# Optimization experiments

Measured on AMD Instinct MI355X. Metric: run time of the kernel, lower is better.

Reference implementation:

```python
import jax, jax.numpy as jnp
import numpy as np

BATCH, SEQ = 4, 2048
D_MODEL, INNER, STATE, K, FFN = 384, 768, 16, 4, 1024


def setup_inputs() -> dict:
    key = jax.random.key(0)
    ks = jax.random.split(key, 12)
    def g(k, shape, scale=0.02):
        return jax.random.normal(k, shape, jnp.float32) * scale
    return {
        "x": jax.random.normal(ks[0], (BATCH, SEQ, D_MODEL), jnp.float32),
        "rms1_w": jnp.ones((D_MODEL,), jnp.float32),
        "rms2_w": jnp.ones((D_MODEL,), jnp.float32),
        "in_proj_w": g(ks[1], (D_MODEL, 2 * INNER)),
        "conv_w": g(ks[2], (K, INNER, INNER)),
        "conv_b": jnp.zeros((INNER,), jnp.float32),
        "x_proj_w": g(ks[3], (INNER, 2 * STATE)),
        "dt_proj_w": g(ks[4], (INNER, INNER)),
        "dt_proj_b": jnp.zeros((INNER,), jnp.float32),
        "A_log": jnp.log(jax.random.uniform(ks[5], (INNER, STATE), jnp.float32, 1.0, 16.0)),
        "D_param": jnp.ones((INNER,), jnp.float32),
        "out_proj_w": g(ks[6], (INNER, D_MODEL)),
        "ln_gamma": jnp.ones((D_MODEL,), jnp.float32),
        "ln_beta": jnp.zeros((D_MODEL,), jnp.float32),
        "gate_w": g(ks[7], (D_MODEL, FFN)),
        "up_w": g(ks[8], (D_MODEL, FFN)),
        "down_w": g(ks[9], (FFN, D_MODEL)),
    }


def rms_norm(x, w, eps=1e-6):
    norm = jnp.sqrt(jnp.mean(jnp.square(x), axis=-1, keepdims=True) + eps)
    return x / norm * w


def layer_norm(x, gamma, beta, eps=1e-5):
    mu = jnp.mean(x, axis=-1, keepdims=True)
    var = jnp.mean(jnp.square(x - mu), axis=-1, keepdims=True)
    return (x - mu) / jnp.sqrt(var + eps) * gamma + beta


def selective_scan(x, delta, A_log, Bm, Cm, Dp):
    # x, delta: [B,L,Di]; Bm, Cm: [B,L,N]; A_log: [Di,N]; Dp: [Di]
    delta = jax.nn.softplus(delta)
    A = -jnp.exp(A_log)                          # [Di,N]
    A_disc = jnp.exp(delta[..., None] * A)       # [B,L,Di,N]
    B_disc = delta[..., None] * Bm[:, :, None, :]  # [B,L,Di,N]
    xs = jnp.moveaxis(x, 1, 0)       # [L,B,Di]
    As = jnp.moveaxis(A_disc, 1, 0)  # [L,B,Di,N]
    Bs = jnp.moveaxis(B_disc, 1, 0)  # [L,B,Di,N]
    Cs = jnp.moveaxis(Cm, 1, 0)      # [L,B,N]
    h0 = jnp.zeros((x.shape[0], A_log.shape[0], A_log.shape[1]), x.dtype)
    def step(h, inp):
        x_t, A_t, B_t, C_t = inp
        h = A_t * h + B_t * x_t[..., None]          # [B,Di,N]
        y_t = jnp.einsum('bdn,bn->bd', h, C_t)      # [B,Di]
        return h, y_t
    _, ys = jax.lax.scan(step, h0, (xs, As, Bs, Cs))
    y = jnp.moveaxis(ys, 0, 1)       # [B,L,Di]
    return y + Dp * x


def mamba_core(h, in_proj_w, conv_w, conv_b, x_proj_w, dt_proj_w, dt_proj_b,
               A_log, D_param, out_proj_w, ln_gamma, ln_beta):
    xz = h @ in_proj_w                             # [B,L,2*Di]
    x_inner, z = jnp.split(xz, 2, axis=-1)
    # Conv1D SAME padding (k=4 -> pad (1,2)), channels-last, kernel [W,I,O]
    x_conv = jax.lax.conv_general_dilated(
        x_inner, conv_w, window_strides=(1,), padding='SAME',
        dimension_numbers=('NWC', 'WIO', 'NWC')) + conv_b
    x_conv = jax.nn.silu(x_conv)
    Bm, Cm = jnp.split(x_conv @ x_proj_w, 2, axis=-1)  # each [B,L,N]
    delta = x_conv @ dt_proj_w + dt_proj_b            # [B,L,Di]
    y = selective_scan(x_conv, delta, A_log, Bm, Cm, D_param)
    y = y * jax.nn.silu(z)
    out = y @ out_proj_w
    return layer_norm(out, ln_gamma, ln_beta)


def reference(x, rms1_w, rms2_w, in_proj_w, conv_w, conv_b, x_proj_w,
              dt_proj_w, dt_proj_b, A_log, D_param, out_proj_w, ln_gamma,
              ln_beta, gate_w, up_w, down_w):
    residual = x
    h = rms_norm(x, rms1_w)
    h = mamba_core(h, in_proj_w, conv_w, conv_b, x_proj_w, dt_proj_w,
                   dt_proj_b, A_log, D_param, out_proj_w, ln_gamma, ln_beta)
    x = residual + h  # dropout inactive (training=False)
    residual = x
    h = rms_norm(x, rms2_w)
    hidden = jax.nn.silu(h @ gate_w) * (h @ up_w)
    x = residual + hidden @ down_w
    return x
```

## Files before the change

### kernel.cpp

```cpp
#include <hip/hip_runtime.h>
#include <hip/hip_bf16.h>


using u16 = unsigned short;
using u32 = unsigned int;
using short8 = __attribute__((ext_vector_type(8))) short;
using f32x4  = __attribute__((ext_vector_type(4))) float;

#define TTOK 8192
#define DM 384
#define DI 768
#define NST 16
#define LSEQ 2048
#define NCH 64
#define LCH 32

#define SWZ_R(row, quad) \
  ((row) * 32 + ((((quad) ^ (row) ^ ((row) >> 2)) & 3) * 8))
#define SWZ_W(tid) SWZ_R((tid) >> 2, (tid) & 3)

__device__ __forceinline__ float bf2f(u16 a) {
  u32 u = ((u32)a) << 16;
  float f; __builtin_memcpy(&f, &u, 4); return f;
}
__device__ __forceinline__ u16 f2bf(float f) {
  u32 u; __builtin_memcpy(&u, &f, 4);
  u32 r = (u + 0x7fffu + ((u >> 16) & 1u)) >> 16;
  return (u16)r;
}
__device__ __forceinline__ int probe_bf(const void* rw) {
  return (((const u32*)rw)[0] == 0x3F803F80u) ? 1 : 0;
}
__device__ __forceinline__ float ld_in(const void* p, int i, int isbf) {
  return isbf ? bf2f(((const u16*)p)[i]) : ((const float*)p)[i];
}
__device__ __forceinline__ float fexp2(float x) {
#if __has_builtin(__builtin_amdgcn_exp2f)
  return __builtin_amdgcn_exp2f(x);
#else
  return exp2f(x);
#endif
}
__device__ __forceinline__ float wave_sum(float v) {
#pragma unroll
  for (int off = 32; off > 0; off >>= 1) v += __shfl_xor(v, off, 64);
  return v;
}

#define V_CB 0
#define V_DB 768
#define V_DP 1536
#define V_R1 2304
#define V_R2 2688
#define V_GA 3072
#define V_BE 3456

__global__ __launch_bounds__(256) void k_prep(
    const void* __restrict__ x, const void* __restrict__ in_proj,
    const void* __restrict__ conv_w, const void* __restrict__ dt_w,
    const void* __restrict__ x_proj, const void* __restrict__ out_proj,
    const void* __restrict__ gate_w, const void* __restrict__ up_w,
    const void* __restrict__ down_w, const void* __restrict__ A_log,
    const void* __restrict__ conv_b, const void* __restrict__ dt_b,
    const void* __restrict__ Dp, const void* __restrict__ rms1_w,
    const void* __restrict__ rms2_w, const void* __restrict__ gamma,
    const void* __restrict__ beta,
    u16* __restrict__ W1T, u16* __restrict__ WCT, u16* __restrict__ W45T,
    u16* __restrict__ W5T, u16* __restrict__ W6T, u16* __restrict__ W7T,
    float* __restrict__ An2T, u16* __restrict__ vecs,
    u16* __restrict__ WinX, u16* __restrict__ h1pad) {
  const int isbf = probe_bf(rms1_w);
  const int bx = blockIdx.x;
  const int tid = threadIdx.x;
  __shared__ u16 lt[64 * 66];

  if (bx < 1236) {
    const void* src; size_t soff = 0; u16* dst; int R, C, tpr, lo;
    if (bx < 144)       { src = in_proj;  dst = W1T;  R = 384;  C = 1536; tpr = 24; lo = bx; }
    else if (bx < 720)  { int tp = (bx - 144) / 144; lo = (bx - 144) % 144;
                          src = conv_w; soff = (size_t)tp * 589824;
                          dst = WCT + (size_t)tp * 589824; R = 768; C = 768; tpr = 12; }
    else if (bx < 864)  { src = dt_w;     dst = W45T; R = 768;  C = 768;  tpr = 12; lo = bx - 720; }
    else if (bx < 876)  { src = x_proj;   dst = W45T + (size_t)768 * 768;
                          R = 768; C = 32; tpr = 1; lo = bx - 864; }
    else if (bx < 948)  { src = out_proj; dst = W5T;  R = 768;  C = 384;  tpr = 6;  lo = bx - 876; }
    else if (bx < 1044) { src = gate_w;   dst = W6T;  R = 384;  C = 1024; tpr = 16; lo = bx - 948; }
    else if (bx < 1140) { src = up_w;     dst = W6T + (size_t)1024 * 384;
                          R = 384; C = 1024; tpr = 16; lo = bx - 1044; }
    else                { src = down_w;   dst = W7T;  R = 1024; C = 384;  tpr = 6;  lo = bx - 1140; }
    int tr = lo / tpr, tc = lo % tpr;
    int r0 = tr * 64, c0 = tc * 64;
#pragma unroll
    for (int i = 0; i < 16; ++i) {
      int el = i * 256 + tid, lr = el >> 6, lc = el & 63;
      if (c0 + lc < C)
        lt[lr * 66 + lc] =
            f2bf(ld_in(src, (int)(soff + (size_t)(r0 + lr) * C + c0 + lc), isbf));
    }
    __syncthreads();
#pragma unroll
    for (int i = 0; i < 16; ++i) {
      int el = i * 256 + tid, orow = el >> 6, oc = el & 63;
      if (c0 + orow < C)
        dst[(size_t)(c0 + orow) * R + r0 + oc] = lt[oc * 66 + orow];
    }
    return;
  }
  if (bx < 5332) {
    int half = tid >> 7;
    int t = (bx - 1236) * 2 + half;
    int tid2 = tid & 127;
    int lane = tid & 63, wv = tid >> 6;
    float v[3]; float q = 0.f;
#pragma unroll
    for (int j = 0; j < 3; ++j) {
      v[j] = ld_in(x, t * DM + tid2 + j * 128, isbf);
      q += v[j] * v[j];
    }
    q = wave_sum(q);
    float* rq = (float*)lt;
    if (lane == 0) rq[wv] = q;
    __syncthreads();
    float rr = rsqrtf((rq[half * 2] + rq[half * 2 + 1]) * (1.f / DM) + 1e-6f);
    int b = t >> 11, l = t & 2047;
    size_t orow = ((size_t)(b * 2051 + l + 1)) * DM;
#pragma unroll
    for (int j = 0; j < 3; ++j) {
      int i = tid2 + j * 128;
      h1pad[orow + i] = f2bf(v[j] * rr * ld_in(rms1_w, i, isbf));
    }
    return;
  }
  if (bx < 6484) {
    int lo = (bx - 5332) * 256 + tid;
    int i = lo / 768, j = lo % 768;
    WinX[lo] = f2bf(ld_in(in_proj, i * 1536 + j, isbf));
    return;
  }
  if (bx < 6532) {
    int lo = (bx - 6484) * 256 + tid;
    if (lo < 12288) {
      int d = lo >> 4, n = lo & 15;
      An2T[n * DI + d] = -__expf(ld_in(A_log, lo, isbf)) * 1.44269504f;
    }
    return;
  }
  if (bx < 6547) {
    int lo = (bx - 6532) * 256 + tid;
    if (lo < 3840) {
      const void* s; int o;
      if      (lo < 768)  { s = conv_b; o = lo; }
      else if (lo < 1536) { s = dt_b;   o = lo - 768; }
      else if (lo < 2304) { s = Dp;     o = lo - 1536; }
      else if (lo < 2688) { s = rms1_w; o = lo - 2304; }
      else if (lo < 3072) { s = rms2_w; o = lo - 2688; }
      else if (lo < 3456) { s = gamma;  o = lo - 3072; }
      else                { s = beta;   o = lo - 3456; }
      vecs[lo] = f2bf(ld_in(s, o, isbf));
    }
    return;
  }
  {
    int lo = (bx - 6547) * 256 + tid;
    if (lo < 4608) {
      int b = lo / (3 * DM), rem = lo % (3 * DM);
      int which = rem / DM, i = rem % DM;
      int row = b * 2051 + (which == 0 ? 0 : (2048 + which));
      h1pad[(size_t)row * DM + i] = 0;
    }
  }
}

__global__ __launch_bounds__(128) void k_lnrms(const float* __restrict__ outm,
                                               const void* __restrict__ xin,
                                               const void* __restrict__ rw,
                                               const u16* __restrict__ vecs,
                                               float* __restrict__ x2f,
                                               u16* __restrict__ h2) {
  const int isbf = probe_bf(rw);
  int t = blockIdx.x, tid = threadIdx.x;
  int lane = tid & 63, wid = tid >> 6;
  float v[3]; float s = 0.f, q = 0.f;
#pragma unroll
  for (int j = 0; j < 3; ++j) {
    v[j] = outm[(size_t)t * DM + tid + j * 128];
    s += v[j]; q += v[j] * v[j];
  }
  s = wave_sum(s); q = wave_sum(q);
  __shared__ float rs[2], rq[2], r2[2];
  if (lane == 0) { rs[wid] = s; rq[wid] = q; }
  __syncthreads();
  float mu = (rs[0] + rs[1]) * (1.f / DM);
  float var = (rq[0] + rq[1]) * (1.f / DM) - mu * mu;
  float rstd = rsqrtf(var + 1e-5f);
  float x2v[3]; float q2 = 0.f;
#pragma unroll
  for (int j = 0; j < 3; ++j) {
    int i = tid + j * 128;
    float ln = (v[j] - mu) * rstd * bf2f(vecs[V_GA + i]) + bf2f(vecs[V_BE + i]);
    x2v[j] = ld_in(xin, t * DM + i, isbf) + ln;
    x2f[(size_t)t * DM + i] = x2v[j];
    q2 += x2v[j] * x2v[j];
  }
  q2 = wave_sum(q2);
  if (lane == 0) r2[wid] = q2;
  __syncthreads();
  float rr = rsqrtf((r2[0] + r2[1]) * (1.f / DM) + 1e-6f);
#pragma unroll
  for (int j = 0; j < 3; ++j) {
    int i = tid + j * 128;
    h2[(size_t)t * DM + i] = f2bf(x2v[j] * rr * bf2f(vecs[V_R2 + i]));
  }
}

template <int EPI, int MT, int NT, int KDIM>
__global__ __launch_bounds__(256) void gemm_bt(
    const u16* __restrict__ A, const u16* __restrict__ BT,
    float* __restrict__ o1, float* __restrict__ o2,
    u16* __restrict__ ob1, u16* __restrict__ ob2,
    const u16* __restrict__ bias, const float* __restrict__ res,
    const void* __restrict__ fl) {
  constexpr int AFR = MT / 32, BFR = NT / 32;
  __shared__ u16 smem[MT * 64 + NT * 64];
  const int tid = threadIdx.x;
  const int lane = tid & 63, wid = tid >> 6;
  const int wm = (wid >> 1) * (MT / 2), wn = (wid & 1) * (NT / 2);
  const int fr = lane & 15, quad = lane >> 4;
  const int r0 = tid >> 2, c8 = (tid & 3) << 3;
  const int m0 = blockIdx.x * MT, n0 = blockIdx.y * NT;

  f32x4 acc[AFR][BFR] = {};

  const u16* BTe = (EPI == 6) ? BT + (size_t)blockIdx.z * 589824 : BT;
  const u16* gB0 = BTe + (size_t)(n0 + r0) * KDIM + c8;
  const u16* gA0 = A + (size_t)(m0 + r0) * KDIM + c8;

  short8 a00, a01, a10, a11, b00, b01, b10, b11;
  auto stage_load = [&](int kt) {
    a00 = *(const short8*)(gA0 + kt);
    a10 = *(const short8*)(gA0 + kt + 32);
    if (MT == 128) {
      a01 = *(const short8*)(gA0 + kt + (size_t)64 * KDIM);
      a11 = *(const short8*)(gA0 + kt + 32 + (size_t)64 * KDIM);
    }
    b00 = *(const short8*)(gB0 + kt);
    b10 = *(const short8*)(gB0 + kt + 32);
    if (NT == 128) {
      b01 = *(const short8*)(gB0 + kt + (size_t)64 * KDIM);
      b11 = *(const short8*)(gB0 + kt + 32 + (size_t)64 * KDIM);
    }
  };

  stage_load(0);

#pragma unroll 1
  for (int kt = 0; kt < KDIM; kt += 64) {
    __syncthreads();
    *(short8*)&smem[SWZ_W(tid)] = a00;
    if (MT == 128) *(short8*)&smem[2048 + SWZ_W(tid)] = a01;
    *(short8*)&smem[MT * 32 + SWZ_W(tid)] = a10;
    if (MT == 128) *(short8*)&smem[MT * 32 + 2048 + SWZ_W(tid)] = a11;
    *(short8*)&smem[MT * 64 + SWZ_W(tid)] = b00;
    if (NT == 128) *(short8*)&smem[MT * 64 + 2048 + SWZ_W(tid)] = b01;
    *(short8*)&smem[MT * 64 + NT * 32 + SWZ_W(tid)] = b10;
    if (NT == 128) *(short8*)&smem[MT * 64 + NT * 32 + 2048 + SWZ_W(tid)] = b11;
    __syncthreads();
    if (kt + 64 < KDIM) stage_load(kt + 64);
#pragma unroll
    for (int kh = 0; kh < 2; ++kh) {
      const int ao = kh * MT * 32, bo = MT * 64 + kh * NT * 32;
      short8 af[AFR], bfg[BFR];
#pragma unroll
      for (int i = 0; i < AFR; ++i)
        af[i] = *(const short8*)&smem[ao + SWZ_R(wm + i * 16 + fr, quad)];
#pragma unroll
      for (int i = 0; i < BFR; ++i)
        bfg[i] = *(const short8*)&smem[bo + SWZ_R(wn + i * 16 + fr, quad)];
#pragma unroll
      for (int mt = 0; mt < AFR; ++mt)
#pragma unroll
        for (int nt = 0; nt < BFR; ++nt)
          acc[mt][nt] = __builtin_amdgcn_mfma_f32_16x16x32_bf16(
              af[mt], bfg[nt], acc[mt][nt], 0, 0, 0);
    }
  }

  int isbf = 0;
  if (EPI == 5) isbf = probe_bf(fl);

#pragma unroll
  for (int mt = 0; mt < AFR; ++mt) {
#pragma unroll
    for (int nt = 0; nt < BFR; ++nt) {
#pragma unroll
      for (int r = 0; r < 4; ++r) {
        int t = m0 + wm + mt * 16 + quad * 4 + r;
        int n = n0 + wn + nt * 16 + fr;
        float v = acc[mt][nt][r];
        if (EPI == 2) {
          if (n < DI) {
            float xx = v + bf2f(bias[n]);
            float sp = (xx > 20.f) ? xx : log1pf(__expf(xx));
            ob1[(size_t)t * DI + n] = f2bf(sp);
          } else if (n < DI + 32) {
            o2[(size_t)t * 32 + (n - DI)] = v;
          }
        } else if (EPI == 3) {
          o1[(size_t)t * DM + n] = v;
        } else if (EPI == 5) {
          float val = v + res[(size_t)t * DM + n];
          if (isbf) ob1[(size_t)t * DM + n] = f2bf(val);
          else      o1[(size_t)t * DM + n] = val;
        } else if (EPI == 6) {
          ob1[(size_t)n * 1536 + blockIdx.z * 384 + t] = f2bf(v);
        }
      }
    }
  }
}

__global__ __launch_bounds__(256) void gemm_xz(
    const u16* __restrict__ A, const u16* __restrict__ WC,
    const u16* __restrict__ WZ, u16* __restrict__ xconv,
    u16* __restrict__ zbuf, const u16* __restrict__ bias) {
  __shared__ u16 smem[8192];
  const int tid = threadIdx.x;
  const int lane = tid & 63, wid = tid >> 6;
  const int wm = (wid >> 1) << 5, wn = (wid & 1) << 5;
  const int fr = lane & 15, quad = lane >> 4;
  const int r0 = tid >> 2, c8 = (tid & 3) << 3;
  const int yb = blockIdx.y;
  const bool isz = yb >= 12;
  const int kd = isz ? 384 : 1536;
  const u16* BT = isz ? WZ : WC;
  const int kldb = isz ? 384 : 1536;
  const int n0 = (isz ? yb - 12 : yb) * 64;
  const int m0 = blockIdx.x * 64;

  f32x4 acc[2][2] = {};

  const u16* gB0 = BT + (size_t)(n0 + r0) * kldb + c8;
  const int b = m0 >> 11, l0 = m0 & 2047;
  const u16* gA0 = A + (size_t)(b * 2051 + l0 + r0 + (isz ? 1 : 0)) * DM + c8;

  short8 a0, a1, b0, b1;
  int wconv = 0, i0 = 0;
  auto calcA = [&]() -> const u16* {
    const u16* p = gA0 + (size_t)wconv * DM + i0;
    i0 += 32;
    if (i0 == DM) { i0 = 0; ++wconv; }
    return p;
  };
  auto stage_load = [&](int kt) {
    a0 = *(const short8*)calcA();
    a1 = *(const short8*)calcA();
    b0 = *(const short8*)(gB0 + kt);
    b1 = *(const short8*)(gB0 + kt + 32);
  };

  stage_load(0);

#pragma unroll 1
  for (int kt = 0; kt < kd; kt += 64) {
    __syncthreads();
    *(short8*)&smem[SWZ_W(tid)]        = a0;
    *(short8*)&smem[2048 + SWZ_W(tid)] = a1;
    *(short8*)&smem[4096 + SWZ_W(tid)] = b0;
    *(short8*)&smem[6144 + SWZ_W(tid)] = b1;
    __syncthreads();
    if (kt + 64 < kd) stage_load(kt + 64);
#pragma unroll
    for (int kh = 0; kh < 2; ++kh) {
      const int ao = kh * 2048, bo = 4096 + kh * 2048;
      short8 af[2], bfg[2];
#pragma unroll
      for (int i = 0; i < 2; ++i)
        af[i] = *(const short8*)&smem[ao + SWZ_R(wm + i * 16 + fr, quad)];
#pragma unroll
      for (int i = 0; i < 2; ++i)
        bfg[i] = *(const short8*)&smem[bo + SWZ_R(wn + i * 16 + fr, quad)];
#pragma unroll
      for (int mt = 0; mt < 2; ++mt)
#pragma unroll
        for (int nt = 0; nt < 2; ++nt)
          acc[mt][nt] = __builtin_amdgcn_mfma_f32_16x16x32_bf16(
              af[mt], bfg[nt], acc[mt][nt], 0, 0, 0);
    }
  }

#pragma unroll
  for (int mt = 0; mt < 2; ++mt) {
#pragma unroll
    for (int nt = 0; nt < 2; ++nt) {
#pragma unroll
      for (int r = 0; r < 4; ++r) {
        int t = m0 + wm + mt * 16 + quad * 4 + r;
        int n = n0 + wn + nt * 16 + fr;
        float v = acc[mt][nt][r];
        if (isz) {
          zbuf[(size_t)t * DI + n] = f2bf(v);
        } else {
          float xx = v + bf2f(bias[n]);
          float sg = 1.f / (1.f + __expf(-xx));
          xconv[(size_t)t * DI + n] = f2bf(xx * sg);
        }
      }
    }
  }
}

__global__ __launch_bounds__(256) void gemm_gu(
    const u16* __restrict__ A, const u16* __restrict__ W6T,
    u16* __restrict__ hid) {
  __shared__ u16 smem[12288];
  const int tid = threadIdx.x;
  const int lane = tid & 63, wid = tid >> 6;
  const int wm = (wid >> 1) << 5, wn = (wid & 1) << 5;
  const int fr = lane & 15, quad = lane >> 4;
  const int r0 = tid >> 2, c8 = (tid & 3) << 3;
  const int m0 = blockIdx.x * 64, n0 = blockIdx.y * 64;

  f32x4 accg[2][2] = {}, accu[2][2] = {};

  const u16* gA0 = A + (size_t)(m0 + r0) * DM + c8;
  const u16* gG0 = W6T + (size_t)(n0 + r0) * DM + c8;
  const u16* gU0 = W6T + (size_t)(1024 + n0 + r0) * DM + c8;

  short8 a0, a1, g00, g10, u00, u10;
  auto stage_load = [&](int kt) {
    a0  = *(const short8*)(gA0 + kt);
    a1  = *(const short8*)(gA0 + kt + 32);
    g00 = *(const short8*)(gG0 + kt);
    g10 = *(const short8*)(gG0 + kt + 32);
    u00 = *(const short8*)(gU0 + kt);
    u10 = *(const short8*)(gU0 + kt + 32);
  };

  stage_load(0);

#pragma unroll 1
  for (int kt = 0; kt < DM; kt += 64) {
    __syncthreads();
    *(short8*)&smem[SWZ_W(tid)]          = a0;
    *(short8*)&smem[2048 + SWZ_W(tid)]   = a1;
    *(short8*)&smem[4096 + SWZ_W(tid)]   = g00;
    *(short8*)&smem[6144 + SWZ_W(tid)]   = g10;
    *(short8*)&smem[8192 + SWZ_W(tid)]   = u00;
    *(short8*)&smem[10240 + SWZ_W(tid)]  = u10;
    __syncthreads();
    if (kt + 64 < DM) stage_load(kt + 64);
#pragma unroll
    for (int kh = 0; kh < 2; ++kh) {
      const int ao = kh * 2048, go = 4096 + kh * 2048, uo = 8192 + kh * 2048;
      short8 af[2], bg[2], bu[2];
#pragma unroll
      for (int i = 0; i < 2; ++i)
        af[i] = *(const short8*)&smem[ao + SWZ_R(wm + i * 16 + fr, quad)];
#pragma unroll
      for (int i = 0; i < 2; ++i) {
        bg[i] = *(const short8*)&smem[go + SWZ_R(wn + i * 16 + fr, quad)];
        bu[i] = *(const short8*)&smem[uo + SWZ_R(wn + i * 16 + fr, quad)];
      }
#pragma unroll
      for (int mt = 0; mt < 2; ++mt)
#pragma unroll
        for (int nt = 0; nt < 2; ++nt) {
          accg[mt][nt] = __builtin_amdgcn_mfma_f32_16x16x32_bf16(
              af[mt], bg[nt], accg[mt][nt], 0, 0, 0);
          accu[mt][nt] = __builtin_amdgcn_mfma_f32_16x16x32_bf16(
              af[mt], bu[nt], accu[mt][nt], 0, 0, 0);
        }
    }
  }

#pragma unroll
  for (int mt = 0; mt < 2; ++mt) {
#pragma unroll
    for (int nt = 0; nt < 2; ++nt) {
#pragma unroll
      for (int r = 0; r < 4; ++r) {
        int t = m0 + wm + mt * 16 + quad * 4 + r;
        int n = n0 + wn + nt * 16 + fr;
        float g = accg[mt][nt][r];
        float u = accu[mt][nt][r];
        float sg = 1.f / (1.f + __expf(-g));
        hid[(size_t)t * 1024 + n] = f2bf(g * sg * u);
      }
    }
  }
}

__global__ __launch_bounds__(256) void k_scan1(
    const u16* __restrict__ deltab, const u16* __restrict__ xconv,
    const float* __restrict__ BC, const float* __restrict__ An2T,
    float* __restrict__ hlb, float* __restrict__ Pb) {
  int gid = blockIdx.x * 256 + threadIdx.x;
  int d = gid % DI, bc = gid / DI, c = bc & (NCH - 1), b = bc >> 6;
  float An[NST];
#pragma unroll
  for (int n = 0; n < NST; ++n) An[n] = An2T[n * DI + d];
  float h[NST], P[NST];
#pragma unroll
  for (int n = 0; n < NST; ++n) { h[n] = 0.f; P[n] = 1.f; }
  int row0 = b * LSEQ + c * LCH;
  float dt = bf2f(deltab[(size_t)row0 * DI + d]);
  float xv = bf2f(xconv[(size_t)row0 * DI + d]);
  float4 q[4];
  {
    const float4* q4 = (const float4*)(BC + (size_t)row0 * 32);
#pragma unroll
    for (int i = 0; i < 4; ++i) q[i] = q4[i];
  }
  for (int s = 0; s < LCH; ++s) {
    float dtc = dt, xvc = xv;
    float Bm[NST];
#pragma unroll
    for (int i = 0; i < 4; ++i) {
      Bm[4*i] = q[i].x; Bm[4*i+1] = q[i].y;
      Bm[4*i+2] = q[i].z; Bm[4*i+3] = q[i].w;
    }
    if (s + 1 < LCH) {
      int r2 = row0 + s + 1;
      dt = bf2f(deltab[(size_t)r2 * DI + d]);
      xv = bf2f(xconv[(size_t)r2 * DI + d]);
      const float4* q4 = (const float4*)(BC + (size_t)r2 * 32);
#pragma unroll
      for (int i = 0; i < 4; ++i) q[i] = q4[i];
    }
    float dxv = dtc * xvc;
#pragma unroll
    for (int n = 0; n < NST; ++n) {
      float a = fexp2(dtc * An[n]);
      h[n] = fmaf(a, h[n], dxv * Bm[n]);
      P[n] *= a;
    }
  }
  float4* ph = (float4*)(hlb + (size_t)gid * NST);
  float4* pp = (float4*)(Pb + (size_t)gid * NST);
#pragma unroll
  for (int i = 0; i < 4; ++i) {
    ph[i] = make_float4(h[4*i], h[4*i+1], h[4*i+2], h[4*i+3]);
    pp[i] = make_float4(P[4*i], P[4*i+1], P[4*i+2], P[4*i+3]);
  }
}

__global__ __launch_bounds__(256) void k_scan2(const float* __restrict__ hlb,
                                               const float* __restrict__ Pb,
                                               float* __restrict__ hin) {
  int gid = blockIdx.x * 256 + threadIdx.x;
  int n = gid & 15, bd = gid >> 4;
  int d = bd % DI, b = bd / DI;
  float H = 0.f;
  for (int c = 0; c < NCH; ++c) {
    size_t idx = ((size_t)((b * NCH + c) * DI + d)) * NST + n;
    hin[idx] = H;
    H = hlb[idx] + Pb[idx] * H;
  }
}

__global__ __launch_bounds__(256) void k_scan3(
    const u16* __restrict__ deltab, const u16* __restrict__ xconv,
    const float* __restrict__ BC, const float* __restrict__ An2T,
    const float* __restrict__ hinb, const u16* __restrict__ zb,
    const u16* __restrict__ vecs, u16* __restrict__ ys) {
  int gid = blockIdx.x * 256 + threadIdx.x;
  int d = gid % DI, bc = gid / DI, c = bc & (NCH - 1), b = bc >> 6;
  float An[NST];
#pragma unroll
  for (int n = 0; n < NST; ++n) An[n] = An2T[n * DI + d];
  float h[NST];
  {
    const float4* hp = (const float4*)(hinb + (size_t)gid * NST);
#pragma unroll
    for (int i = 0; i < 4; ++i) {
      float4 t = hp[i];
      h[4*i] = t.x; h[4*i+1] = t.y; h[4*i+2] = t.z; h[4*i+3] = t.w;
    }
  }
  float Dd = bf2f(vecs[V_DP + d]);
  int row0 = b * LSEQ + c * LCH;
  float dt = bf2f(deltab[(size_t)row0 * DI + d]);
  float xv = bf2f(xconv[(size_t)row0 * DI + d]);
  float zv = bf2f(zb[(size_t)row0 * DI + d]);
  float4 q[8];
  {
    const float4* q4 = (const float4*)(BC + (size_t)row0 * 32);
#pragma unroll
    for (int i = 0; i < 8; ++i) q[i] = q4[i];
  }
  for (int s = 0; s < LCH; ++s) {
    int row = row0 + s;
    float dtc = dt, xvc = xv, zvc = zv;
    float Bm[NST], Cm[NST];
#pragma unroll
    for (int i = 0; i < 4; ++i) {
      Bm[4*i] = q[i].x;   Bm[4*i+1] = q[i].y;
      Bm[4*i+2] = q[i].z; Bm[4*i+3] = q[i].w;
      Cm[4*i] = q[4+i].x;   Cm[4*i+1] = q[4+i].y;
      Cm[4*i+2] = q[4+i].z; Cm[4*i+3] = q[4+i].w;
    }
    if (s + 1 < LCH) {
      int r2 = row + 1;
      dt = bf2f(deltab[(size_t)r2 * DI + d]);
      xv = bf2f(xconv[(size_t)r2 * DI + d]);
      zv = bf2f(zb[(size_t)r2 * DI + d]);
      const float4* q4 = (const float4*)(BC + (size_t)r2 * 32);
#pragma unroll
      for (int i = 0; i < 8; ++i) q[i] = q4[i];
    }
    float dxv = dtc * xvc;
    float yp[4] = {0.f, 0.f, 0.f, 0.f};
#pragma unroll
    for (int n = 0; n < NST; ++n) {
      float a = fexp2(dtc * An[n]);
      h[n] = fmaf(a, h[n], dxv * Bm[n]);
      yp[n & 3] = fmaf(h[n], Cm[n], yp[n & 3]);
    }
    float y = (yp[0] + yp[1]) + (yp[2] + yp[3]);
    float sz = zvc / (1.f + __expf(-zvc));
    ys[(size_t)row * DI + d] = f2bf((y + Dd * xvc) * sz);
  }
}

extern "C" void kernel_launch(void* const* d_in, const int* in_sizes, int n_in,
                              void* d_out, int out_size, void* d_ws,
                              size_t ws_size, hipStream_t stream) {
  (void)in_sizes; (void)n_in; (void)out_size;
  const void* x        = d_in[0];
  const void* rms1_w   = d_in[1];
  const void* rms2_w   = d_in[2];
  const void* in_proj  = d_in[3];
  const void* conv_w   = d_in[4];
  const void* conv_b   = d_in[5];
  const void* x_proj   = d_in[6];
  const void* dt_w     = d_in[7];
  const void* dt_b     = d_in[8];
  const void* A_log    = d_in[9];
  const void* Dp       = d_in[10];
  const void* out_proj = d_in[11];
  const void* gamma    = d_in[12];
  const void* beta     = d_in[13];
  const void* gate_w   = d_in[14];
  const void* up_w     = d_in[15];
  const void* down_w   = d_in[16];

  char* ws = (char*)d_ws;
  size_t off = 0;
  auto alloc = [&](size_t bytes) -> void* {
    void* p = ws + off;
    off = (off + bytes + 255) & ~(size_t)255;
    return p;
  };
  u16*   W1T   = (u16*)alloc((size_t)1536 * 384 * 2);
  u16*   WCT   = (u16*)alloc((size_t)4 * 768 * 768 * 2);
  u16*   W45T  = (u16*)alloc((size_t)896 * 768 * 2);
  u16*   W5T   = (u16*)alloc((size_t)384 * 768 * 2);
  u16*   W6T   = (u16*)alloc((size_t)2048 * 384 * 2);
  u16*   W7T   = (u16*)alloc((size_t)384 * 1024 * 2);
  float* An2T  = (float*)alloc((size_t)16 * 768 * 4);
  u16*   vecs  = (u16*)alloc(3840 * 2);
  u16*   WinX  = (u16*)alloc((size_t)384 * 768 * 2);
  u16*   WcombT= (u16*)alloc((size_t)768 * 1536 * 2);
  u16*   h1pad = (u16*)alloc((size_t)4 * 2051 * 384 * 2);
  u16*   zbuf  = (u16*)alloc((size_t)8192 * 768 * 2);
  u16*   xconv = (u16*)alloc((size_t)8192 * 768 * 2);
  u16*   deltab= (u16*)alloc((size_t)8192 * 768 * 2);
  float* BCb   = (float*)alloc((size_t)8192 * 32 * 4);
  float* hl    = (float*)alloc((size_t)196608 * 16 * 4);
  float* Pb    = (float*)alloc((size_t)196608 * 16 * 4);
  float* hin   = (float*)alloc((size_t)196608 * 16 * 4);
  u16*   ys   = (u16*)hl;
  float* outm = Pb;
  float* x2f  = hin;
  u16*   h2   = h1pad;
  u16*   hid  = (u16*)hl;

  if (off > ws_size) return;

  k_prep<<<6565, 256, 0, stream>>>(
      x, in_proj, conv_w, dt_w, x_proj, out_proj, gate_w, up_w, down_w,
      A_log, conv_b, dt_b, Dp, rms1_w, rms2_w, gamma, beta,
      W1T, WCT, W45T, W5T, W6T, W7T, An2T, vecs, WinX, h1pad);

  gemm_bt<6, 64, 64, 768><<<dim3(6, 12, 4), 256, 0, stream>>>(
      WinX, WCT, nullptr, nullptr, WcombT, nullptr, nullptr, nullptr, nullptr);

  gemm_xz<<<dim3(128, 24), 256, 0, stream>>>(
      h1pad, WcombT, W1T + (size_t)768 * 384, xconv, zbuf, vecs + V_CB);

  gemm_bt<2, 64, 64, 768><<<dim3(128, 13), 256, 0, stream>>>(
      xconv, W45T, nullptr, BCb, deltab, nullptr, vecs + V_DB, nullptr,
      nullptr);

  k_scan1<<<768, 256, 0, stream>>>(deltab, xconv, BCb, An2T, hl, Pb);
  k_scan2<<<192, 256, 0, stream>>>(hl, Pb, hin);
  k_scan3<<<768, 256, 0, stream>>>(deltab, xconv, BCb, An2T, hin, zbuf, vecs,
                                   ys);

  gemm_bt<3, 64, 64, 768><<<dim3(128, 6), 256, 0, stream>>>(
      ys, W5T, outm, nullptr, nullptr, nullptr, nullptr, nullptr, nullptr);
  k_lnrms<<<8192, 128, 0, stream>>>(outm, x, rms1_w, vecs, x2f, h2);

  gemm_gu<<<dim3(128, 16), 256, 0, stream>>>(h2, W6T, hid);
  gemm_bt<5, 64, 64, 1024><<<dim3(128, 6), 256, 0, stream>>>(
      hid, W7T, (float*)d_out, nullptr, (u16*)d_out, nullptr, nullptr, x2f,
      rms1_w);
}
```

Measured before the change: 323.8 us.

## Use direct global-to-LDS loads with double-buffered shared memory in GEMMs

Replaces the register-staged global loads in gemm_bt and gemm_xz with global_load_lds DMA-style copies straight into LDS, and double-buffers shared memory so the next tile loads while the current one is consumed. This drops one __syncthreads per k-step and the VGPR round-trip for staging data. It doubles LDS use per block and relies on the swizzle computed on the source side plus implicit wait semantics; there is no explicit vmcnt wait before the barrier, which could be a correctness risk depending on compiler handling.

```diff
diff --git a/kernel.cpp b/kernel.cpp
--- a/kernel.cpp
+++ b/kernel.cpp
@@ -45,6 +45,12 @@
 #pragma unroll
   for (int off = 32; off > 0; off >>= 1) v += __shfl_xor(v, off, 64);
   return v;
+}
+
+__device__ __forceinline__ void gl_lds16(const u16* g, u16* l) {
+  __builtin_amdgcn_global_load_lds(
+      (const __attribute__((address_space(1))) u32*)g,
+      (__attribute__((address_space(3))) u32*)l, 16, 0, 0);
 }
 
 #define V_CB 0
@@ -213,85 +219,72 @@
   }
 }
 
-template <int EPI, int MT, int NT, int KDIM>
+template <int EPI, int KDIM>
 __global__ __launch_bounds__(256) void gemm_bt(
     const u16* __restrict__ A, const u16* __restrict__ BT,
     float* __restrict__ o1, float* __restrict__ o2,
     u16* __restrict__ ob1, u16* __restrict__ ob2,
     const u16* __restrict__ bias, const float* __restrict__ res,
     const void* __restrict__ fl) {
-  constexpr int AFR = MT / 32, BFR = NT / 32;
-  __shared__ u16 smem[MT * 64 + NT * 64];
+  __shared__ u16 smem[2][8192];
   const int tid = threadIdx.x;
   const int lane = tid & 63, wid = tid >> 6;
-  const int wm = (wid >> 1) * (MT / 2), wn = (wid & 1) * (NT / 2);
+  const int wm = (wid >> 1) << 5, wn = (wid & 1) << 5;
   const int fr = lane & 15, quad = lane >> 4;
-  const int r0 = tid >> 2, c8 = (tid & 3) << 3;
-  const int m0 = blockIdx.x * MT, n0 = blockIdx.y * NT;
-
-  f32x4 acc[AFR][BFR] = {};
-
+  const int m0 = blockIdx.x * 64, n0 = blockIdx.y * 64;
+
+  f32x4 acc[2][2] = {};
+
+  const int wrow = (wid << 4) | (lane >> 2);
+  const int sq = ((lane & 3) ^ wrow ^ (wrow >> 2)) & 3;
   const u16* BTe = (EPI == 6) ? BT + (size_t)blockIdx.z * 589824 : BT;
-  const u16* gB0 = BTe + (size_t)(n0 + r0) * KDIM + c8;
-  const u16* gA0 = A + (size_t)(m0 + r0) * KDIM + c8;
-
-  short8 a00, a01, a10, a11, b00, b01, b10, b11;
-  auto stage_load = [&](int kt) {
-    a00 = *(const short8*)(gA0 + kt);
-    a10 = *(const short8*)(gA0 + kt + 32);
-    if (MT == 128) {
-      a01 = *(const short8*)(gA0 + kt + (size_t)64 * KDIM);
-      a11 = *(const short8*)(gA0 + kt + 32 + (size_t)64 * KDIM);
-    }
-    b00 = *(const short8*)(gB0 + kt);
-    b10 = *(const short8*)(gB0 + kt + 32);
-    if (NT == 128) {
-      b01 = *(const short8*)(gB0 + kt + (size_t)64 * KDIM);
-      b11 = *(const short8*)(gB0 + kt + 32 + (size_t)64 * KDIM);
-    }
+  const u16* srcA = A + (size_t)(m0 + wrow) * KDIM + sq * 8;
+  const u16* srcB = BTe + (size_t)(n0 + wrow) * KDIM + sq * 8;
+  u16* lw = &smem[0][0] + (wid << 9);
+
+  auto stage = [&](int buf, int kt) {
+    u16* lb = lw + buf * 8192;
+    gl_lds16(srcA + kt,      lb);
+    gl_lds16(srcA + kt + 32, lb + 2048);
+    gl_lds16(srcB + kt,      lb + 4096);
+    gl_lds16(srcB + kt + 32, lb + 6144);
   };
 
-  stage_load(0);
+  stage(0, 0);
+  int cur = 0;
 
 #pragma unroll 1
   for (int kt = 0; kt < KDIM; kt += 64) {
     __syncthreads();
-    *(short8*)&smem[SWZ_W(tid)] = a00;
-    if (MT == 128) *(short8*)&smem[2048 + SWZ_W(tid)] = a01;
-    *(short8*)&smem[MT * 32 + SWZ_W(tid)] = a10;
-    if (MT == 128) *(short8*)&smem[MT * 32 + 2048 + SWZ_W(tid)] = a11;
-    *(short8*)&smem[MT * 64 + SWZ_W(tid)] = b00;
-    if (NT == 128) *(short8*)&smem[MT * 64 + 2048 + SWZ_W(tid)] = b01;
-    *(short8*)&smem[MT * 64 + NT * 32 + SWZ_W(tid)] = b10;
-    if (NT == 128) *(short8*)&smem[MT * 64 + NT * 32 + 2048 + SWZ_W(tid)] = b11;
-    __syncthreads();
-    if (kt + 64 < KDIM) stage_load(kt + 64);
+    if (kt + 64 < KDIM) stage(cur ^ 1, kt + 64);
+    const u16* sm = &smem[cur][0];
 #pragma unroll
     for (int kh = 0; kh < 2; ++kh) {
-      const int ao = kh * MT * 32, bo = MT * 64 + kh * NT * 32;
-      short8 af[AFR], bfg[BFR];
-#pragma unroll
-      for (int i = 0; i < AFR; ++i)
-        af[i] = *(const short8*)&smem[ao + SWZ_R(wm + i * 16 + fr, quad)];
-#pragma unroll
-      for (int i = 0; i < BFR; ++i)
-        bfg[i] = *(const short8*)&smem[bo + SWZ_R(wn + i * 16 + fr, quad)];
-#pragma unroll
-      for (int mt = 0; mt < AFR; ++mt)
-#pragma unroll
-        for (int nt = 0; nt < BFR; ++nt)
+      const int ao = kh * 2048, bo = 4096 + kh * 2048;
+      short8 af[2], bfg[2];
+#pragma unroll
+      for (int i = 0; i < 2; ++i)
+        af[i] = *(const short8*)&sm[ao + SWZ_R(wm + i * 16 + fr, quad)];
+#pragma unroll
+      for (int i = 0; i < 2; ++i)
+        bfg[i] = *(const short8*)&sm[bo + SWZ_R(wn + i * 16 + fr, quad)];
+#pragma unroll
+      for (int mt = 0; mt < 2; ++mt)
+#pragma unroll
+        for (int nt = 0; nt < 2; ++nt)
           acc[mt][nt] = __builtin_amdgcn_mfma_f32_16x16x32_bf16(
               af[mt], bfg[nt], acc[mt][nt], 0, 0, 0);
     }
+    cur ^= 1;
   }
 
   int isbf = 0;
   if (EPI == 5) isbf = probe_bf(fl);
 
 #pragma unroll
-  for (int mt = 0; mt < AFR; ++mt) {
-#pragma unroll
-    for (int nt = 0; nt < BFR; ++nt) {
+  for (int mt = 0; mt < 2; ++mt) {
+#pragma unroll
+    for (int nt = 0; nt < 2; ++nt) {
 #pragma unroll
       for (int r = 0; r < 4; ++r) {
         int t = m0 + wm + mt * 16 + quad * 4 + r;
@@ -323,12 +316,11 @@
     const u16* __restrict__ A, const u16* __restrict__ WC,
     const u16* __restrict__ WZ, u16* __restrict__ xconv,
     u16* __restrict__ zbuf, const u16* __restrict__ bias) {
-  __shared__ u16 smem[8192];
+  __shared__ u16 smem[2][8192];
   const int tid = threadIdx.x;
   const int lane = tid & 63, wid = tid >> 6;
   const int wm = (wid >> 1) << 5, wn = (wid & 1) << 5;
   const int fr = lane & 15, quad = lane >> 4;
-  const int r0 = tid >> 2, c8 = (tid & 3) << 3;
   const int yb = blockIdx.y;
   const bool isz = yb >= 12;
   const int kd = isz ? 384 : 1536;
@@ -339,46 +331,43 @@
 
   f32x4 acc[2][2] = {};
 
-  const u16* gB0 = BT + (size_t)(n0 + r0) * kldb + c8;
+  const int wrow = (wid << 4) | (lane >> 2);
+  const int sq = ((lane & 3) ^ wrow ^ (wrow >> 2)) & 3;
+  const u16* srcB = BT + (size_t)(n0 + wrow) * kldb + sq * 8;
   const int b = m0 >> 11, l0 = m0 & 2047;
-  const u16* gA0 = A + (size_t)(b * 2051 + l0 + r0 + (isz ? 1 : 0)) * DM + c8;
-
-  short8 a0, a1, b0, b1;
-  int wconv = 0, i0 = 0;
-  auto calcA = [&]() -> const u16* {
-    const u16* p = gA0 + (size_t)wconv * DM + i0;
-    i0 += 32;
-    if (i0 == DM) { i0 = 0; ++wconv; }
-    return p;
+  const u16* srcA0 =
+      A + (size_t)(b * 2051 + l0 + wrow + (isz ? 1 : 0)) * DM + sq * 8;
+  u16* lw = &smem[0][0] + (wid << 9);
+
+  int wc = 0, ic = 0;
+  auto stage = [&](int buf, int kt) {
+    u16* lb = lw + buf * 8192;
+    const u16* sa = srcA0 + (size_t)wc * DM + ic;
+    gl_lds16(sa,           lb);
+    gl_lds16(sa + 32,      lb + 2048);
+    gl_lds16(srcB + kt,      lb + 4096);
+    gl_lds16(srcB + kt + 32, lb + 6144);
+    ic += 64; if (ic == 384) { ic = 0; ++wc; }
   };
-  auto stage_load = [&](int kt) {
-    a0 = *(const short8*)calcA();
-    a1 = *(const short8*)calcA();
-    b0 = *(const short8*)(gB0 + kt);
-    b1 = *(const short8*)(gB0 + kt + 32);
-  };
-
-  stage_load(0);
+
+  stage(0, 0);
+  int cur = 0;
 
 #pragma unroll 1
   for (int kt = 0; kt < kd; kt += 64) {
     __syncthreads();
-    *(short8*)&smem[SWZ_W(tid)]        = a0;
-    *(short8*)&smem[2048 + SWZ_W(tid)] = a1;
-    *(short8*)&smem[4096 + SWZ_W(tid)] = b0;
-    *(short8*)&smem[6144 + SWZ_W(tid)] = b1;
-    __syncthreads();
-    if (kt + 64 < kd) stage_load(kt + 64);
+    if (kt + 64 < kd) stage(cur ^ 1, kt + 64);
+    const u16* sm = &smem[cur][0];
 #pragma unroll
     for (int kh = 0; kh < 2; ++kh) {
       const int ao = kh * 2048, bo = 4096 + kh * 2048;
       short8 af[2], bfg[2];
 #pragma unroll
       for (int i = 0; i < 2; ++i)
-        af[i] = *(const short8*)&smem[ao + SWZ_R(wm + i * 16 + fr, quad)];
+        af[i] = *(const short8*)&sm[ao + SWZ_R(wm + i * 16 + fr, quad)];
 #pragma unroll
       for (int i = 0; i < 2; ++i)
-        bfg[i] = *(const short8*)&smem[bo + SWZ_R(wn + i * 16 + fr, quad)];
+        bfg[i] = *(const short8*)&sm[bo + SWZ_R(wn + i * 16 + fr, quad)];
 #pragma unroll
       for (int mt = 0; mt < 2; ++mt)
 #pragma unroll
@@ -386,6 +375,7 @@
           acc[mt][nt] = __builtin_amdgcn_mfma_f32_16x16x32_bf16(
               af[mt], bfg[nt], acc[mt][nt], 0, 0, 0);
     }
+    cur ^= 1;
   }
 
 #pragma unroll
@@ -682,13 +672,13 @@
       A_log, conv_b, dt_b, Dp, rms1_w, rms2_w, gamma, beta,
       W1T, WCT, W45T, W5T, W6T, W7T, An2T, vecs, WinX, h1pad);
 
-  gemm_bt<6, 64, 64, 768><<<dim3(6, 12, 4), 256, 0, stream>>>(
+  gemm_bt<6, 768><<<dim3(6, 12, 4), 256, 0, stream>>>(
       WinX, WCT, nullptr, nullptr, WcombT, nullptr, nullptr, nullptr, nullptr);
 
   gemm_xz<<<dim3(128, 24), 256, 0, stream>>>(
       h1pad, WcombT, W1T + (size_t)768 * 384, xconv, zbuf, vecs + V_CB);
 
-  gemm_bt<2, 64, 64, 768><<<dim3(128, 13), 256, 0, stream>>>(
+  gemm_bt<2, 768><<<dim3(128, 13), 256, 0, stream>>>(
       xconv, W45T, nullptr, BCb, deltab, nullptr, vecs + V_DB, nullptr,
       nullptr);
 
@@ -697,12 +687,12 @@
   k_scan3<<<768, 256, 0, stream>>>(deltab, xconv, BCb, An2T, hin, zbuf, vecs,
                                    ys);
 
-  gemm_bt<3, 64, 64, 768><<<dim3(128, 6), 256, 0, stream>>>(
+  gemm_bt<3, 768><<<dim3(128, 6), 256, 0, stream>>>(
       ys, W5T, outm, nullptr, nullptr, nullptr, nullptr, nullptr, nullptr);
   k_lnrms<<<8192, 128, 0, stream>>>(outm, x, rms1_w, vecs, x2f, h2);
 
   gemm_gu<<<dim3(128, 16), 256, 0, stream>>>(h2, W6T, hid);
-  gemm_bt<5, 64, 64, 1024><<<dim3(128, 6), 256, 0, stream>>>(
+  gemm_bt<5, 1024><<<dim3(128, 6), 256, 0, stream>>>(
       hid, W7T, (float*)d_out, nullptr, (u16*)d_out, nullptr, nullptr, x2f,
       rms1_w);
 }
```

New measurement: 320.6 us. Within noise of the previous version (-1.0%).
